# Optimization experiments

Hardware: AMD Instinct MI355X
Metric: run time of the kernel (lower is better)

## Reference

```python
import jax, jax.numpy as jnp
import numpy as np

B, T, D = 1024, 512, 64   # batch, seq_len, input_dim
H, L, OUT = 8, 3, 1       # hidden (mid_dim), num_layers, output_dim


def setup_inputs() -> dict:
    key = jax.random.key(0)
    ks = jax.random.split(key, 18)
    s = 1.0 / np.sqrt(H)  # torch LSTM default init scale
    u = lambda k, shape: jax.random.uniform(k, shape, jnp.float32, -s, s)
    return {
        "input_seq": jax.random.normal(ks[0], (B, T, D), jnp.float32),
        "h0": jax.random.normal(ks[1], (L, B, H), jnp.float32),
        "c0": jax.random.normal(ks[2], (L, B, H), jnp.float32),
        # encoder LSTM params (layer0 input dim differs)
        "enc_Wih0": u(ks[3], (4 * H, D)),
        "enc_Wih_rest": u(ks[4], (L - 1, 4 * H, H)),
        "enc_Whh": u(ks[5], (L, 4 * H, H)),
        "enc_bih": u(ks[6], (L, 4 * H)),
        "enc_bhh": u(ks[7], (L, 4 * H)),
        # decoder LSTM params
        "dec_Wih0": u(ks[8], (4 * H, D)),
        "dec_Wih_rest": u(ks[9], (L - 1, 4 * H, H)),
        "dec_Whh": u(ks[10], (L, 4 * H, H)),
        "dec_bih": u(ks[11], (L, 4 * H)),
        "dec_bhh": u(ks[12], (L, 4 * H)),
        # decoder output projection
        "lin_W": u(ks[13], (OUT, H)),
        "lin_b": u(ks[14], (OUT,)),
    }


def _cell(x, h, c, Wih, Whh, b):
    # one LSTM cell step, torch gate order: i, f, g, o
    gates = x @ Wih.T + h @ Whh.T + b  # [B, 4H]
    i, f, g, o = jnp.split(gates, 4, axis=-1)
    c2 = jax.nn.sigmoid(f) * c + jax.nn.sigmoid(i) * jnp.tanh(g)
    h2 = jax.nn.sigmoid(o) * jnp.tanh(c2)
    return h2, c2


def _stack_step(h, c, x_t, Wih0, Wih_rest, Whh, bih, bhh):
    # one timestep through all L layers; h, c: [L, B, H]
    hs, cs = [], []
    inp = x_t
    for l in range(L):
        Wih = Wih0 if l == 0 else Wih_rest[l - 1]
        h_l, c_l = _cell(inp, h[l], c[l], Wih, Whh[l], bih[l] + bhh[l])
        hs.append(h_l)
        cs.append(c_l)
        inp = h_l
    return jnp.stack(hs), jnp.stack(cs)


def reference(input_seq, h0, c0, enc_Wih0, enc_Wih_rest, enc_Whh, enc_bih, enc_bhh,
              dec_Wih0, dec_Wih_rest, dec_Whh, dec_bih, dec_bhh, lin_W, lin_b):
    x_tbd = jnp.transpose(input_seq, (1, 0, 2))  # [T, B, D] for scan

    # Encoder: full-sequence 3-layer LSTM, keep final (h, c)
    def enc_step(carry, x_t):
        h, c = carry
        h2, c2 = _stack_step(h, c, x_t, enc_Wih0, enc_Wih_rest, enc_Whh, enc_bih, enc_bhh)
        return (h2, c2), None

    (h, c), _ = jax.lax.scan(enc_step, (h0, c0), x_tbd)

    # Decoder: one LSTM step per timestep, fed the input at that step
    def dec_step(carry, x_t):
        h, c = carry
        h2, c2 = _stack_step(h, c, x_t, dec_Wih0, dec_Wih_rest, dec_Whh, dec_bih, dec_bhh)
        return (h2, c2), None

    (h, c), _ = jax.lax.scan(dec_step, (h, c), x_tbd)

    # original returns outputs[:, -1, :] = linear applied to last decoder output
    pred_last = h[-1] @ lin_W.T + lin_b  # [B, OUT]
    return pred_last
```

## Files before the change

### kernel.cpp

```cpp
#include <hip/hip_runtime.h>

#define TT 512
#define DD 64
#define BB 1024
#define PF 8
#define HH 8

__device__ __forceinline__ float fexp2(float x){ return __builtin_amdgcn_exp2f(x); }
__device__ __forceinline__ float frcp (float x){ return __builtin_amdgcn_rcpf(x); }

template<int C>
__device__ __forceinline__ float dppf(float x){
  return __int_as_float(__builtin_amdgcn_update_dpp(0, __float_as_int(x), C, 0xF, 0xF, true));
}
template<int C>
__device__ __forceinline__ int dppi(int x){
  return __builtin_amdgcn_update_dpp(0, x, C, 0xF, 0xF, true);
}

__device__ __forceinline__ float swz16(float x){
  return __int_as_float(__builtin_amdgcn_ds_swizzle(__float_as_int(x), 0x401F));
}

template<int N> struct IC { static constexpr int v = N; };

__global__ __launch_bounds__(256) void proj_kernel(
    const float* __restrict__ x,
    const float* __restrict__ eWih0, const float* __restrict__ eBih, const float* __restrict__ eBhh,
    const float* __restrict__ dWih0, const float* __restrict__ dBih, const float* __restrict__ dBhh,
    float* __restrict__ P)
{
  __shared__ __align__(16) float xs[4][2][16 * 64];
  const int tid  = threadIdx.x;
  const int w    = tid >> 6;
  const int lane = tid & 63;
  const int rsel = lane >> 5;
  const int j    = lane & 31;
  const int ph   = j >> 4;
  const int m    = j & 15;
  const int r_even = (m >> 2) * 8 + (m & 3);
  const int r_odd  = r_even + 4;

  const float* W  = ph ? dWih0 : eWih0;
  const float* Bi = ph ? dBih  : eBih;
  const float* Bh = ph ? dBhh  : eBhh;
  const float bA = Bi[r_even] + Bh[r_even];
  const float bB = Bi[r_odd]  + Bh[r_odd];

  float Wa[64], Wb[64];
#pragma unroll
  for (int k = 0; k < 16; ++k) {
    float4 wq = *(const float4*)(W + r_even * 64 + k * 4);
    Wa[k*4+0] = wq.x; Wa[k*4+1] = wq.y; Wa[k*4+2] = wq.z; Wa[k*4+3] = wq.w;
  }
#pragma unroll
  for (int k = 0; k < 16; ++k) {
    float4 wq = *(const float4*)(W + r_odd * 64 + k * 4);
    Wb[k*4+0] = wq.x; Wb[k*4+1] = wq.y; Wb[k*4+2] = wq.z; Wb[k*4+3] = wq.w;
  }

  const int base_row = (blockIdx.x * 4 + w) * 64;
  const float* xg = x + (size_t)base_row * 64;

  float4 st[4];
#pragma unroll
  for (int i = 0; i < 4; ++i) st[i] = *(const float4*)(xg + i * 256 + lane * 4);
#pragma unroll
  for (int i = 0; i < 4; ++i) *(float4*)&xs[w][0][i * 256 + lane * 4] = st[i];
#pragma unroll
  for (int i = 0; i < 4; ++i) st[i] = *(const float4*)(xg + 1024 + i * 256 + lane * 4);

#pragma unroll 1
  for (int g = 0; g < 4; ++g) {
    const float* buf = &xs[w][g & 1][0];
#pragma unroll 2
    for (int ci = 0; ci < 8; ++ci) {
      const int rib = ci * 2 + rsel;
      const float* xr = buf + rib * 64;
      float a0A = bA, a1A = 0.f, a2A = 0.f, a3A = 0.f;
      float a0B = bB, a1B = 0.f, a2B = 0.f, a3B = 0.f;
#pragma unroll
      for (int kc = 0; kc < 16; ++kc) {
        float4 xv = *(const float4*)(xr + kc * 4);
        a0A = fmaf(Wa[kc*4+0], xv.x, a0A);
        a1A = fmaf(Wa[kc*4+1], xv.y, a1A);
        a2A = fmaf(Wa[kc*4+2], xv.z, a2A);
        a3A = fmaf(Wa[kc*4+3], xv.w, a3A);
        a0B = fmaf(Wb[kc*4+0], xv.x, a0B);
        a1B = fmaf(Wb[kc*4+1], xv.y, a1B);
        a2B = fmaf(Wb[kc*4+2], xv.z, a2B);
        a3B = fmaf(Wb[kc*4+3], xv.w, a3B);
      }
      const int row = base_row + g * 16 + rib;
      const int e = row >> 9, t = row & 511;
      float2 res; res.x = (a0A + a1A) + (a2A + a3A);
                  res.y = (a0B + a1B) + (a2B + a3B);
      *(float2*)(P + ((size_t)((ph << 10) + e) * TT + t) * 32 + 2 * m) = res;
    }
    if (g < 3) {
#pragma unroll
      for (int i = 0; i < 4; ++i) *(float4*)&xs[w][(g + 1) & 1][i * 256 + lane * 4] = st[i];
      if (g < 2) {
#pragma unroll
        for (int i = 0; i < 4; ++i)
          st[i] = *(const float4*)(xg + (size_t)(g + 2) * 1024 + i * 256 + lane * 4);
      }
    }
  }
}

__global__ __launch_bounds__(128) void recur_kernel(
    const float* __restrict__ P,
    const float* __restrict__ h0,    const float* __restrict__ c0,
    const float* __restrict__ eWihR, const float* __restrict__ eWhh,
    const float* __restrict__ eBih,  const float* __restrict__ eBhh,
    const float* __restrict__ dWihR, const float* __restrict__ dWhh,
    const float* __restrict__ dBih,  const float* __restrict__ dBhh,
    const float* __restrict__ linW,  const float* __restrict__ linB,
    float* __restrict__ out)
{
  const int tid = threadIdx.x;
  const int idx = tid & 31;
  const int v   = idx >> 2;
  const int g   = idx & 3;
  const int b   = v & 3;
  const bool rB = (v >= 4);
  const int e   = blockIdx.x * 4 + (tid >> 5);

  const bool is_tanh = (g == 2);
  const float ns_act = is_tanh ? -2.885390082f : -1.44269504f;
  const float a_act  = is_tanh ? 2.0f : 1.0f;
  const float b_act  = is_tanh ? -1.0f : 0.0f;

  const int qidx = (tid >> 2) & 3;
  const int p4 = dppi<0x124>(qidx);
  const int d  = __builtin_amdgcn_readfirstlane((p4 - qidx) & 3);

  float H[3], cs[3], sd[3];
  float bd1 = 0.f, bd2 = 0.f;
  float WS[3][8], WB[2][8], Bss[2];

#pragma unroll
  for (int l = 0; l < 3; ++l) {
    H[l]  = h0[((size_t)l * BB + e) * HH + v];
    cs[l] = c0[((size_t)l * BB + e) * HH + v];
  }

  auto bcast = [&](float hn, float* A, float* Bv) {
    float Hsw = swz16(hn);
    float Lo = rB ? Hsw : hn;
    float Hi = rB ? hn : Hsw;
    A[0]  = Lo; A[1]  = dppf<0x124>(Lo); A[2]  = dppf<0x128>(Lo); A[3]  = dppf<0x12C>(Lo);
    Bv[0] = Hi; Bv[1] = dppf<0x124>(Hi); Bv[2] = dppf<0x128>(Hi); Bv[3] = dppf<0x12C>(Hi);
  };

  auto load_phase = [&](const float* WihR, const float* Whh,
                        const float* Bih, const float* Bhh) {
#pragma unroll
    for (int l = 0; l < 3; ++l) {
      const int r0 = l * 32 + g * 8 + v;
#pragma unroll
      for (int k = 0; k < 4; ++k) {
        const int col = (b + d * k) & 3;
        WS[l][k]     = Whh[r0 * 8 + col];
        WS[l][4 + k] = Whh[r0 * 8 + 4 + col];
      }
    }
#pragma unroll
    for (int l = 0; l < 2; ++l) {
      const int r0 = l * 32 + g * 8 + v;
#pragma unroll
      for (int k = 0; k < 4; ++k) {
        const int col = (b + d * k) & 3;
        WB[l][k]     = WihR[r0 * 8 + col];
        WB[l][4 + k] = WihR[r0 * 8 + 4 + col];
      }
      Bss[l] = Bih[(l + 1) * 32 + g * 8 + v] + Bhh[(l + 1) * 32 + g * 8 + v];
    }
#pragma unroll
    for (int l = 0; l < 3; ++l) {
      float A[4], Bv[4];
      bcast(H[l], A, Bv);
      float acc = l ? Bss[l - 1] : 0.f;
#pragma unroll
      for (int k = 0; k < 4; ++k) {
        acc = fmaf(WS[l][k],     A[k],  acc);
        acc = fmaf(WS[l][4 + k], Bv[k], acc);
      }
      sd[l] = acc;
    }
  };

  auto lstep = [&](auto LC, float in) -> float {
    constexpr int l = decltype(LC)::v;
    float pre = in + sd[l];
    float ex  = fexp2(ns_act * pre);
    float rc  = frcp(1.f + ex);
    float act = fmaf(a_act, rc, b_act);
    float Gi = dppf<0x00>(act);
    float Gf = dppf<0x55>(act);
    float Gg = dppf<0xAA>(act);
    float Go = dppf<0xFF>(act);
    float cn = fmaf(Gf, cs[l], Gi * Gg);
    cs[l] = cn;
    float tx = fexp2(-2.885390082f * cn);
    float tr = frcp(1.f + tx);
    float th = fmaf(2.f, tr, -1.f);
    float hn = Go * th;
    H[l] = hn;
    float A[4], Bv[4];
    bcast(hn, A, Bv);
    float accS;
    if constexpr (l > 0) accS = Bss[l - 1]; else accS = 0.f;
#pragma unroll
    for (int k = 0; k < 4; ++k) {
      accS = fmaf(WS[l][k],     A[k],  accS);
      accS = fmaf(WS[l][4 + k], Bv[k], accS);
    }
    sd[l] = accS;
    float accB = 0.f;
    if constexpr (l < 2) {
#pragma unroll
      for (int k = 0; k < 4; ++k) {
        accB = fmaf(WB[l][k],     A[k],  accB);
        accB = fmaf(WB[l][4 + k], Bv[k], accB);
      }
    }
    return accB;
  };

  auto lstep3 = [&](float in0, float in1, float in2, float& nb1, float& nb2) {
    float pre0 = in0 + sd[0];
    float pre1 = in1 + sd[1];
    float pre2 = in2 + sd[2];
    float ex0 = fexp2(ns_act * pre0);
    float ex1 = fexp2(ns_act * pre1);
    float ex2 = fexp2(ns_act * pre2);
    float rc0 = frcp(1.f + ex0);
    float rc1 = frcp(1.f + ex1);
    float rc2 = frcp(1.f + ex2);
    float ac0 = fmaf(a_act, rc0, b_act);
    float ac1 = fmaf(a_act, rc1, b_act);
    float ac2 = fmaf(a_act, rc2, b_act);
    float Gi0 = dppf<0x00>(ac0), Gi1 = dppf<0x00>(ac1), Gi2 = dppf<0x00>(ac2);
    float Gf0 = dppf<0x55>(ac0), Gf1 = dppf<0x55>(ac1), Gf2 = dppf<0x55>(ac2);
    float Gg0 = dppf<0xAA>(ac0), Gg1 = dppf<0xAA>(ac1), Gg2 = dppf<0xAA>(ac2);
    float Go0 = dppf<0xFF>(ac0), Go1 = dppf<0xFF>(ac1), Go2 = dppf<0xFF>(ac2);
    float cn0 = fmaf(Gf0, cs[0], Gi0 * Gg0);
    float cn1 = fmaf(Gf1, cs[1], Gi1 * Gg1);
    float cn2 = fmaf(Gf2, cs[2], Gi2 * Gg2);
    cs[0] = cn0; cs[1] = cn1; cs[2] = cn2;
    float tx0 = fexp2(-2.885390082f * cn0);
    float tx1 = fexp2(-2.885390082f * cn1);
    float tx2 = fexp2(-2.885390082f * cn2);
    float tr0 = frcp(1.f + tx0);
    float tr1 = frcp(1.f + tx1);
    float tr2 = frcp(1.f + tx2);
    float th0 = fmaf(2.f, tr0, -1.f);
    float th1 = fmaf(2.f, tr1, -1.f);
    float th2 = fmaf(2.f, tr2, -1.f);
    float hn0 = Go0 * th0;
    float hn1 = Go1 * th1;
    float hn2 = Go2 * th2;
    H[0] = hn0; H[1] = hn1; H[2] = hn2;
    float sw0 = swz16(hn0);
    float sw1 = swz16(hn1);
    float sw2 = swz16(hn2);
    float Lo0 = rB ? sw0 : hn0, Hi0 = rB ? hn0 : sw0;
    float Lo1 = rB ? sw1 : hn1, Hi1 = rB ? hn1 : sw1;
    float Lo2 = rB ? sw2 : hn2, Hi2 = rB ? hn2 : sw2;
    float A0[4], B0[4], A1[4], B1[4], A2[4], B2[4];
    A0[0] = Lo0; A0[1] = dppf<0x124>(Lo0); A0[2] = dppf<0x128>(Lo0); A0[3] = dppf<0x12C>(Lo0);
    B0[0] = Hi0; B0[1] = dppf<0x124>(Hi0); B0[2] = dppf<0x128>(Hi0); B0[3] = dppf<0x12C>(Hi0);
    A1[0] = Lo1; A1[1] = dppf<0x124>(Lo1); A1[2] = dppf<0x128>(Lo1); A1[3] = dppf<0x12C>(Lo1);
    B1[0] = Hi1; B1[1] = dppf<0x124>(Hi1); B1[2] = dppf<0x128>(Hi1); B1[3] = dppf<0x12C>(Hi1);
    A2[0] = Lo2; A2[1] = dppf<0x124>(Lo2); A2[2] = dppf<0x128>(Lo2); A2[3] = dppf<0x12C>(Lo2);
    B2[0] = Hi2; B2[1] = dppf<0x124>(Hi2); B2[2] = dppf<0x128>(Hi2); B2[3] = dppf<0x12C>(Hi2);
    float s0 = 0.f, s1 = Bss[0], s2 = Bss[1];
    float u0 = 0.f, u1 = 0.f;
#pragma unroll
    for (int k = 0; k < 4; ++k) {
      s0 = fmaf(WS[0][k],     A0[k], s0);
      s0 = fmaf(WS[0][4 + k], B0[k], s0);
      s1 = fmaf(WS[1][k],     A1[k], s1);
      s1 = fmaf(WS[1][4 + k], B1[k], s1);
      s2 = fmaf(WS[2][k],     A2[k], s2);
      s2 = fmaf(WS[2][4 + k], B2[k], s2);
      u0 = fmaf(WB[0][k],     A0[k], u0);
      u0 = fmaf(WB[0][4 + k], B0[k], u0);
      u1 = fmaf(WB[1][k],     A1[k], u1);
      u1 = fmaf(WB[1][4 + k], B1[k], u1);
    }
    sd[0] = s0; sd[1] = s1; sd[2] = s2;
    nb1 = u0; nb2 = u1;
  };

#pragma unroll 1
  for (int ph = 0; ph < 2; ++ph) {
    if (ph == 0) load_phase(eWihR, eWhh, eBih, eBhh);
    else         load_phase(dWihR, dWhh, dBih, dBhh);

    const int pos = (g * 4 + b) * 2 + (v >> 2);
    const float* Pb = P + ((size_t)((ph << 10) + e) * TT) * 32 + pos;

    float pf[PF];
#pragma unroll
    for (int k = 0; k < PF; ++k) pf[k] = Pb[k * 32];

#pragma unroll
    for (int k = 0; k < PF; ++k) {
      float cur = pf[k];
      pf[k] = Pb[(k + PF) * 32];
      float n1 = lstep(IC<0>{}, cur);
      float n2 = 0.f;
      if (k >= 1) n2 = lstep(IC<1>{}, bd1);
      if (k >= 2) (void)lstep(IC<2>{}, bd2);
      bd1 = n1; bd2 = n2;
    }

#pragma unroll 1
    for (int t = PF; t < TT - PF; t += PF) {
      const float* Pq = Pb + (size_t)(t + PF) * 32;
#pragma unroll
      for (int k = 0; k < PF; ++k) {
        float cur = pf[k];
        pf[k] = Pq[k * 32];
        float n1, n2;
        lstep3(cur, bd1, bd2, n1, n2);
        bd1 = n1; bd2 = n2;
      }
    }
#pragma unroll
    for (int k = 0; k < PF; ++k) {
      float cur = pf[k];
      float n1, n2;
      lstep3(cur, bd1, bd2, n1, n2);
      bd1 = n1; bd2 = n2;
    }

    float dd = lstep(IC<1>{}, bd1);
    (void)lstep(IC<2>{}, bd2);
    (void)lstep(IC<2>{}, dd);
  }

  float lwA[4], lwB[4];
#pragma unroll
  for (int k = 0; k < 4; ++k) {
    const int col = (b + d * k) & 3;
    lwA[k] = linW[col];
    lwB[k] = linW[4 + col];
  }
  float A[4], Bv[4];
  bcast(H[2], A, Bv);
  float pred = linB[0];
#pragma unroll
  for (int k = 0; k < 4; ++k) {
    pred = fmaf(lwA[k], A[k],  pred);
    pred = fmaf(lwB[k], Bv[k], pred);
  }
  if (idx == 0) out[e] = pred;
}

__global__ __launch_bounds__(64) void seq2seq_fallback(
    const float* __restrict__ x, const float* __restrict__ h0, const float* __restrict__ c0,
    const float* __restrict__ eWih0, const float* __restrict__ eWihR, const float* __restrict__ eWhh,
    const float* __restrict__ eBih,  const float* __restrict__ eBhh,
    const float* __restrict__ dWih0, const float* __restrict__ dWihR, const float* __restrict__ dWhh,
    const float* __restrict__ dBih,  const float* __restrict__ dBhh,
    const float* __restrict__ linW,  const float* __restrict__ linB, float* __restrict__ out)
{
  const int tid = threadIdx.x;
  const int g   = tid & 31;
  const int grp = tid & 32;
  const int jj  = g & 7;
  const int e   = blockIdx.x * 2 + (tid >> 5);
  const bool is_tanh = ((g >> 3) == 2);
  const float s_act = is_tanh ? 2.885390082f : 1.44269504f;
  const float a_act = is_tanh ? 2.0f : 1.0f;
  const float b_act = is_tanh ? -1.0f : 0.0f;
  float hrep[3][8]; float cc[3];
#pragma unroll
  for (int l = 0; l < 3; ++l) {
#pragma unroll
    for (int k = 0; k < 8; ++k) hrep[l][k] = h0[((size_t)l * BB + e) * HH + k];
    cc[l] = c0[((size_t)l * BB + e) * HH + jj];
  }
  for (int p = 0; p < 2; ++p) {
    const float* Wih0 = p ? dWih0 : eWih0;  const float* WihR = p ? dWihR : eWihR;
    const float* Whh  = p ? dWhh  : eWhh;   const float* Bih  = p ? dBih  : eBih;
    const float* Bhh  = p ? dBhh  : eBhh;
    float Wx[64];
#pragma unroll
    for (int k = 0; k < 64; k += 4) {
      float4 w = *(const float4*)(Wih0 + g * 64 + k);
      Wx[k] = w.x; Wx[k+1] = w.y; Wx[k+2] = w.z; Wx[k+3] = w.w;
    }
    float Wh[3][8], Wi[2][8], bias[3];
#pragma unroll
    for (int l = 0; l < 3; ++l) {
#pragma unroll
      for (int k = 0; k < 8; ++k) Wh[l][k] = Whh[(l*32+g)*8+k];
      bias[l] = Bih[l*32+g] + Bhh[l*32+g];
    }
#pragma unroll
    for (int l = 0; l < 2; ++l)
#pragma unroll
      for (int k = 0; k < 8; ++k) Wi[l][k] = WihR[(l*32+g)*8+k];
    const float* xrow = x + (size_t)e * TT * DD;
    for (int t = 0; t < TT; ++t) {
      float4 acc = make_float4(bias[0], 0.f, 0.f, 0.f);
#pragma unroll
      for (int kc = 0; kc < 16; ++kc) {
        float4 xv = *(const float4*)(xrow + kc * 4);
        acc.x = fmaf(Wx[kc*4+0], xv.x, acc.x); acc.y = fmaf(Wx[kc*4+1], xv.y, acc.y);
        acc.z = fmaf(Wx[kc*4+2], xv.z, acc.z); acc.w = fmaf(Wx[kc*4+3], xv.w, acc.w);
      }
      float pre = (acc.x + acc.y) + (acc.z + acc.w);
      { float r0=0.f,r1=0.f;
#pragma unroll
        for (int k = 0; k < 8; k += 2) { r0=fmaf(Wh[0][k],hrep[0][k],r0); r1=fmaf(Wh[0][k+1],hrep[0][k+1],r1); }
        pre += r0 + r1; }
#pragma unroll
      for (int l = 0; l < 3; ++l) {
        if (l > 0) {
          float r0 = bias[l], r1 = 0.f;
#pragma unroll
          for (int k = 0; k < 8; k += 2) {
            r0=fmaf(Wi[l-1][k],hrep[l-1][k],r0); r1=fmaf(Wi[l-1][k+1],hrep[l-1][k+1],r1);
            r0=fmaf(Wh[l][k],hrep[l][k],r0);     r1=fmaf(Wh[l][k+1],hrep[l][k+1],r1);
          }
          pre = r0 + r1;
        }
        float act = fmaf(a_act, frcp(1.0f + fexp2(-s_act * pre)), b_act);
        float iv = __shfl(act, grp + jj);
        float fv = __shfl(act, grp + 8 + jj);
        float gv = __shfl(act, grp + 16 + jj);
        float ov = __shfl(act, grp + 24 + jj);
        float cn = fmaf(fv, cc[l], iv * gv);
        cc[l] = cn;
        float th = fmaf(2.0f, frcp(1.0f + fexp2(-2.885390082f * cn)), -1.0f);
        float hn = ov * th;
#pragma unroll
        for (int k = 0; k < 8; ++k) hrep[l][k] = __shfl(hn, grp + k);
      }
      xrow += DD;
    }
  }
  float pred = linB[0];
#pragma unroll
  for (int k = 0; k < 8; ++k) pred = fmaf(linW[k], hrep[2][k], pred);
  if (g == 0) out[e] = pred;
}

extern "C" void kernel_launch(void* const* d_in, const int* in_sizes, int n_in,
                              void* d_out, int out_size, void* d_ws, size_t ws_size,
                              hipStream_t stream) {
  const float* x     = (const float*)d_in[0];
  const float* h0    = (const float*)d_in[1];
  const float* c0    = (const float*)d_in[2];
  const float* eWih0 = (const float*)d_in[3];
  const float* eWihR = (const float*)d_in[4];
  const float* eWhh  = (const float*)d_in[5];
  const float* eBih  = (const float*)d_in[6];
  const float* eBhh  = (const float*)d_in[7];
  const float* dWih0 = (const float*)d_in[8];
  const float* dWihR = (const float*)d_in[9];
  const float* dWhh  = (const float*)d_in[10];
  const float* dBih  = (const float*)d_in[11];
  const float* dBhh  = (const float*)d_in[12];
  const float* linW  = (const float*)d_in[13];
  const float* linB  = (const float*)d_in[14];
  float* out = (float*)d_out;

  const size_t P_BYTES = (size_t)2 * BB * TT * 32 * sizeof(float);
  if (ws_size >= P_BYTES) {
    float* P = (float*)d_ws;
    proj_kernel<<<2048, 256, 0, stream>>>(x, eWih0, eBih, eBhh, dWih0, dBih, dBhh, P);
    recur_kernel<<<BB / 4, 128, 0, stream>>>(P, h0, c0, eWihR, eWhh, eBih, eBhh,
                                             dWihR, dWhh, dBih, dBhh, linW, linB, out);
  } else {
    seq2seq_fallback<<<BB / 2, 64, 0, stream>>>(x, h0, c0, eWih0, eWihR, eWhh, eBih, eBhh,
                                                dWih0, dWihR, dWhh, dBih, dBhh, linW, linB, out);
  }
}
```

Measured before the change: 573.8 us.

## Fuse input projection into recurrence kernel with producer/consumer waves via LDS

Replaces the separate projection kernel and its global workspace with one fused kernel. Two waves per block compute the layer-0 input projection for 32-timestep windows into double-buffered LDS, while the other two waves run the LSTM recurrence, with a block barrier at each window boundary. This removes the large global write and read-back of the projected gates and one kernel launch. The cost is 96KB of LDS per block, a barrier every window, and consumer waves that may stall if producers fall behind. The fallback kernel is removed.

```diff
diff --git a/kernel.cpp b/kernel.cpp
--- a/kernel.cpp
+++ b/kernel.cpp
@@ -5,6 +5,8 @@
 #define BB 1024
 #define PF 8
 #define HH 8
+#define WBLK 32
+#define NWIN (TT / WBLK)
 
 __device__ __forceinline__ float fexp2(float x){ return __builtin_amdgcn_exp2f(x); }
 __device__ __forceinline__ float frcp (float x){ return __builtin_amdgcn_rcpf(x); }
@@ -24,108 +26,32 @@
 
 template<int N> struct IC { static constexpr int v = N; };
 
-__global__ __launch_bounds__(256) void proj_kernel(
+__global__ __launch_bounds__(256) void fused_kernel(
     const float* __restrict__ x,
-    const float* __restrict__ eWih0, const float* __restrict__ eBih, const float* __restrict__ eBhh,
-    const float* __restrict__ dWih0, const float* __restrict__ dBih, const float* __restrict__ dBhh,
-    float* __restrict__ P)
-{
-  __shared__ __align__(16) float xs[4][2][16 * 64];
-  const int tid  = threadIdx.x;
-  const int w    = tid >> 6;
-  const int lane = tid & 63;
-  const int rsel = lane >> 5;
-  const int j    = lane & 31;
-  const int ph   = j >> 4;
-  const int m    = j & 15;
-  const int r_even = (m >> 2) * 8 + (m & 3);
-  const int r_odd  = r_even + 4;
-
-  const float* W  = ph ? dWih0 : eWih0;
-  const float* Bi = ph ? dBih  : eBih;
-  const float* Bh = ph ? dBhh  : eBhh;
-  const float bA = Bi[r_even] + Bh[r_even];
-  const float bB = Bi[r_odd]  + Bh[r_odd];
-
-  float Wa[64], Wb[64];
-#pragma unroll
-  for (int k = 0; k < 16; ++k) {
-    float4 wq = *(const float4*)(W + r_even * 64 + k * 4);
-    Wa[k*4+0] = wq.x; Wa[k*4+1] = wq.y; Wa[k*4+2] = wq.z; Wa[k*4+3] = wq.w;
-  }
-#pragma unroll
-  for (int k = 0; k < 16; ++k) {
-    float4 wq = *(const float4*)(W + r_odd * 64 + k * 4);
-    Wb[k*4+0] = wq.x; Wb[k*4+1] = wq.y; Wb[k*4+2] = wq.z; Wb[k*4+3] = wq.w;
-  }
-
-  const int base_row = (blockIdx.x * 4 + w) * 64;
-  const float* xg = x + (size_t)base_row * 64;
-
-  float4 st[4];
-#pragma unroll
-  for (int i = 0; i < 4; ++i) st[i] = *(const float4*)(xg + i * 256 + lane * 4);
-#pragma unroll
-  for (int i = 0; i < 4; ++i) *(float4*)&xs[w][0][i * 256 + lane * 4] = st[i];
-#pragma unroll
-  for (int i = 0; i < 4; ++i) st[i] = *(const float4*)(xg + 1024 + i * 256 + lane * 4);
-
-#pragma unroll 1
-  for (int g = 0; g < 4; ++g) {
-    const float* buf = &xs[w][g & 1][0];
-#pragma unroll 2
-    for (int ci = 0; ci < 8; ++ci) {
-      const int rib = ci * 2 + rsel;
-      const float* xr = buf + rib * 64;
-      float a0A = bA, a1A = 0.f, a2A = 0.f, a3A = 0.f;
-      float a0B = bB, a1B = 0.f, a2B = 0.f, a3B = 0.f;
-#pragma unroll
-      for (int kc = 0; kc < 16; ++kc) {
-        float4 xv = *(const float4*)(xr + kc * 4);
-        a0A = fmaf(Wa[kc*4+0], xv.x, a0A);
-        a1A = fmaf(Wa[kc*4+1], xv.y, a1A);
-        a2A = fmaf(Wa[kc*4+2], xv.z, a2A);
-        a3A = fmaf(Wa[kc*4+3], xv.w, a3A);
-        a0B = fmaf(Wb[kc*4+0], xv.x, a0B);
-        a1B = fmaf(Wb[kc*4+1], xv.y, a1B);
-        a2B = fmaf(Wb[kc*4+2], xv.z, a2B);
-        a3B = fmaf(Wb[kc*4+3], xv.w, a3B);
-      }
-      const int row = base_row + g * 16 + rib;
-      const int e = row >> 9, t = row & 511;
-      float2 res; res.x = (a0A + a1A) + (a2A + a3A);
-                  res.y = (a0B + a1B) + (a2B + a3B);
-      *(float2*)(P + ((size_t)((ph << 10) + e) * TT + t) * 32 + 2 * m) = res;
-    }
-    if (g < 3) {
-#pragma unroll
-      for (int i = 0; i < 4; ++i) *(float4*)&xs[w][(g + 1) & 1][i * 256 + lane * 4] = st[i];
-      if (g < 2) {
-#pragma unroll
-        for (int i = 0; i < 4; ++i)
-          st[i] = *(const float4*)(xg + (size_t)(g + 2) * 1024 + i * 256 + lane * 4);
-      }
-    }
-  }
-}
-
-__global__ __launch_bounds__(128) void recur_kernel(
-    const float* __restrict__ P,
     const float* __restrict__ h0,    const float* __restrict__ c0,
-    const float* __restrict__ eWihR, const float* __restrict__ eWhh,
+    const float* __restrict__ eWih0, const float* __restrict__ eWihR, const float* __restrict__ eWhh,
     const float* __restrict__ eBih,  const float* __restrict__ eBhh,
-    const float* __restrict__ dWihR, const float* __restrict__ dWhh,
+    const float* __restrict__ dWih0, const float* __restrict__ dWihR, const float* __restrict__ dWhh,
     const float* __restrict__ dBih,  const float* __restrict__ dBhh,
     const float* __restrict__ linW,  const float* __restrict__ linB,
     float* __restrict__ out)
 {
-  const int tid = threadIdx.x;
+  extern __shared__ __align__(16) float smem[];
+  float* Pbuf = smem;
+  float* xst  = smem + 2 * WBLK * 4 * 32;
+
+  const int tid  = threadIdx.x;
+  const int wv   = tid >> 6;
+  const int lane = tid & 63;
+  const bool prod = (wv >= 2);
+
   const int idx = tid & 31;
   const int v   = idx >> 2;
   const int g   = idx & 3;
   const int b   = v & 3;
   const bool rB = (v >= 4);
-  const int e   = blockIdx.x * 4 + (tid >> 5);
+  const int erow = tid >> 5;
+  const int e    = blockIdx.x * 4 + erow;
 
   const bool is_tanh = (g == 2);
   const float ns_act = is_tanh ? -2.885390082f : -1.44269504f;
@@ -138,13 +64,23 @@
 
   float H[3], cs[3], sd[3];
   float bd1 = 0.f, bd2 = 0.f;
-  float WS[3][8], WB[2][8], Bss[2];
-
-#pragma unroll
-  for (int l = 0; l < 3; ++l) {
-    H[l]  = h0[((size_t)l * BB + e) * HH + v];
-    cs[l] = c0[((size_t)l * BB + e) * HH + v];
+  float WS[3][8], WBr[2][8], Bss[2];
+
+  if (!prod) {
+#pragma unroll
+    for (int l = 0; l < 3; ++l) {
+      H[l]  = h0[((size_t)l * BB + e) * HH + v];
+      cs[l] = c0[((size_t)l * BB + e) * HH + v];
+    }
   }
+
+  const int rsel = lane >> 4;
+  const int m    = lane & 15;
+  const int r_even = (m >> 2) * 8 + (m & 3);
+  const int r_odd  = r_even + 4;
+  const int p0 = (wv - 2) * 2;
+  float Wa[64], Wb[64];
+  float bA = 0.f, bB = 0.f;
 
   auto bcast = [&](float hn, float* A, float* Bv) {
     float Hsw = swz16(hn);
@@ -172,8 +108,8 @@
 #pragma unroll
       for (int k = 0; k < 4; ++k) {
         const int col = (b + d * k) & 3;
-        WB[l][k]     = WihR[r0 * 8 + col];
-        WB[l][4 + k] = WihR[r0 * 8 + 4 + col];
+        WBr[l][k]     = WihR[r0 * 8 + col];
+        WBr[l][4 + k] = WihR[r0 * 8 + 4 + col];
       }
       Bss[l] = Bih[(l + 1) * 32 + g * 8 + v] + Bhh[(l + 1) * 32 + g * 8 + v];
     }
@@ -222,8 +158,8 @@
     if constexpr (l < 2) {
 #pragma unroll
       for (int k = 0; k < 4; ++k) {
-        accB = fmaf(WB[l][k],     A[k],  accB);
-        accB = fmaf(WB[l][4 + k], Bv[k], accB);
+        accB = fmaf(WBr[l][k],     A[k],  accB);
+        accB = fmaf(WBr[l][4 + k], Bv[k], accB);
       }
     }
     return accB;
@@ -286,170 +222,163 @@
       s1 = fmaf(WS[1][4 + k], B1[k], s1);
       s2 = fmaf(WS[2][k],     A2[k], s2);
       s2 = fmaf(WS[2][4 + k], B2[k], s2);
-      u0 = fmaf(WB[0][k],     A0[k], u0);
-      u0 = fmaf(WB[0][4 + k], B0[k], u0);
-      u1 = fmaf(WB[1][k],     A1[k], u1);
-      u1 = fmaf(WB[1][4 + k], B1[k], u1);
+      u0 = fmaf(WBr[0][k],     A0[k], u0);
+      u0 = fmaf(WBr[0][4 + k], B0[k], u0);
+      u1 = fmaf(WBr[1][k],     A1[k], u1);
+      u1 = fmaf(WBr[1][4 + k], B1[k], u1);
     }
     sd[0] = s0; sd[1] = s1; sd[2] = s2;
     nb1 = u0; nb2 = u1;
   };
 
-#pragma unroll 1
-  for (int ph = 0; ph < 2; ++ph) {
-    if (ph == 0) load_phase(eWihR, eWhh, eBih, eBhh);
-    else         load_phase(dWihR, dWhh, dBih, dBhh);
-
-    const int pos = (g * 4 + b) * 2 + (v >> 2);
-    const float* Pb = P + ((size_t)((ph << 10) + e) * TT) * 32 + pos;
-
+  const int pos_c = (g * 4 + b) * 2 + (v >> 2);
+
+  auto consume = [&](int w) {
+    const float* Pw = Pbuf + ((w & 1) * WBLK * 4 * 32) + erow * 32 + pos_c;
     float pf[PF];
 #pragma unroll
-    for (int k = 0; k < PF; ++k) pf[k] = Pb[k * 32];
-
-#pragma unroll
-    for (int k = 0; k < PF; ++k) {
-      float cur = pf[k];
-      pf[k] = Pb[(k + PF) * 32];
-      float n1 = lstep(IC<0>{}, cur);
-      float n2 = 0.f;
-      if (k >= 1) n2 = lstep(IC<1>{}, bd1);
-      if (k >= 2) (void)lstep(IC<2>{}, bd2);
-      bd1 = n1; bd2 = n2;
-    }
-
-#pragma unroll 1
-    for (int t = PF; t < TT - PF; t += PF) {
-      const float* Pq = Pb + (size_t)(t + PF) * 32;
+    for (int k = 0; k < PF; ++k) pf[k] = Pw[k * 128];
+    if (w == 0) {
 #pragma unroll
       for (int k = 0; k < PF; ++k) {
         float cur = pf[k];
-        pf[k] = Pq[k * 32];
-        float n1, n2;
-        lstep3(cur, bd1, bd2, n1, n2);
+        pf[k] = Pw[(PF + k) * 128];
+        float n1 = lstep(IC<0>{}, cur);
+        float n2 = 0.f;
+        if (k >= 1) n2 = lstep(IC<1>{}, bd1);
+        if (k >= 2) (void)lstep(IC<2>{}, bd2);
         bd1 = n1; bd2 = n2;
       }
-    }
-#pragma unroll
-    for (int k = 0; k < PF; ++k) {
-      float cur = pf[k];
+#pragma unroll 1
+      for (int gi = 1; gi < 3; ++gi) {
+#pragma unroll
+        for (int j = 0; j < PF; ++j) {
+          float cur = pf[j];
+          pf[j] = Pw[((gi + 1) * PF + j) * 128];
+          float n1, n2;
+          lstep3(cur, bd1, bd2, n1, n2);
+          bd1 = n1; bd2 = n2;
+        }
+      }
+    } else {
+#pragma unroll 1
+      for (int gi = 0; gi < 3; ++gi) {
+#pragma unroll
+        for (int j = 0; j < PF; ++j) {
+          float cur = pf[j];
+          pf[j] = Pw[((gi + 1) * PF + j) * 128];
+          float n1, n2;
+          lstep3(cur, bd1, bd2, n1, n2);
+          bd1 = n1; bd2 = n2;
+        }
+      }
+    }
+#pragma unroll
+    for (int j = 0; j < PF; ++j) {
+      float cur = pf[j];
       float n1, n2;
       lstep3(cur, bd1, bd2, n1, n2);
       bd1 = n1; bd2 = n2;
     }
-
-    float dd = lstep(IC<1>{}, bd1);
-    (void)lstep(IC<2>{}, bd2);
-    (void)lstep(IC<2>{}, dd);
+  };
+
+  auto produce = [&](int w, int buf) {
+#pragma unroll 1
+    for (int es = 0; es < 2; ++es) {
+      const int p  = p0 + es;
+      const float* xg = x + ((size_t)(blockIdx.x * 4 + p) * TT + w * WBLK) * 64;
+      float* xp = xst + p * (WBLK * 64);
+      float4 sv[8];
+#pragma unroll
+      for (int i = 0; i < 8; ++i) sv[i] = *(const float4*)(xg + i * 256 + lane * 4);
+#pragma unroll
+      for (int i = 0; i < 8; ++i) *(float4*)(xp + i * 256 + lane * 4) = sv[i];
+#pragma unroll 1
+      for (int ci = 0; ci < 8; ++ci) {
+        const int rib = ci * 4 + rsel;
+        const float* xr = xp + rib * 64;
+        float a0A = bA, a1A = 0.f, a2A = 0.f, a3A = 0.f;
+        float a0B = bB, a1B = 0.f, a2B = 0.f, a3B = 0.f;
+#pragma unroll
+        for (int kc = 0; kc < 16; ++kc) {
+          float4 xv = *(const float4*)(xr + kc * 4);
+          a0A = fmaf(Wa[kc*4+0], xv.x, a0A);
+          a1A = fmaf(Wa[kc*4+1], xv.y, a1A);
+          a2A = fmaf(Wa[kc*4+2], xv.z, a2A);
+          a3A = fmaf(Wa[kc*4+3], xv.w, a3A);
+          a0B = fmaf(Wb[kc*4+0], xv.x, a0B);
+          a1B = fmaf(Wb[kc*4+1], xv.y, a1B);
+          a2B = fmaf(Wb[kc*4+2], xv.z, a2B);
+          a3B = fmaf(Wb[kc*4+3], xv.w, a3B);
+        }
+        float2 res;
+        res.x = (a0A + a1A) + (a2A + a3A);
+        res.y = (a0B + a1B) + (a2B + a3B);
+        *(float2*)(Pbuf + ((size_t)(buf * WBLK + rib) * 4 + p) * 32 + 2 * m) = res;
+      }
+    }
+  };
+
+#pragma unroll 1
+  for (int ph = 0; ph < 2; ++ph) {
+    if (prod) {
+      const float* W  = ph ? dWih0 : eWih0;
+      const float* Bi = ph ? dBih  : eBih;
+      const float* Bh = ph ? dBhh  : eBhh;
+      bA = Bi[r_even] + Bh[r_even];
+      bB = Bi[r_odd]  + Bh[r_odd];
+#pragma unroll
+      for (int k = 0; k < 16; ++k) {
+        float4 wq = *(const float4*)(W + r_even * 64 + k * 4);
+        Wa[k*4+0] = wq.x; Wa[k*4+1] = wq.y; Wa[k*4+2] = wq.z; Wa[k*4+3] = wq.w;
+      }
+#pragma unroll
+      for (int k = 0; k < 16; ++k) {
+        float4 wq = *(const float4*)(W + r_odd * 64 + k * 4);
+        Wb[k*4+0] = wq.x; Wb[k*4+1] = wq.y; Wb[k*4+2] = wq.z; Wb[k*4+3] = wq.w;
+      }
+      produce(0, 0);
+    } else {
+      if (ph == 0) load_phase(eWihR, eWhh, eBih, eBhh);
+      else         load_phase(dWihR, dWhh, dBih, dBhh);
+    }
+    __syncthreads();
+
+#pragma unroll 1
+    for (int w = 0; w < NWIN; ++w) {
+      if (prod) {
+        if (w < NWIN - 1) produce(w + 1, (w + 1) & 1);
+      } else {
+        consume(w);
+      }
+      __syncthreads();
+    }
+
+    if (!prod) {
+      float dd = lstep(IC<1>{}, bd1);
+      (void)lstep(IC<2>{}, bd2);
+      (void)lstep(IC<2>{}, dd);
+    }
   }
 
-  float lwA[4], lwB[4];
-#pragma unroll
-  for (int k = 0; k < 4; ++k) {
-    const int col = (b + d * k) & 3;
-    lwA[k] = linW[col];
-    lwB[k] = linW[4 + col];
+  if (!prod) {
+    float lwA[4], lwB[4];
+#pragma unroll
+    for (int k = 0; k < 4; ++k) {
+      const int col = (b + d * k) & 3;
+      lwA[k] = linW[col];
+      lwB[k] = linW[4 + col];
+    }
+    float A[4], Bv[4];
+    bcast(H[2], A, Bv);
+    float pred = linB[0];
+#pragma unroll
+    for (int k = 0; k < 4; ++k) {
+      pred = fmaf(lwA[k], A[k],  pred);
+      pred = fmaf(lwB[k], Bv[k], pred);
+    }
+    if (idx == 0) out[e] = pred;
   }
-  float A[4], Bv[4];
-  bcast(H[2], A, Bv);
-  float pred = linB[0];
-#pragma unroll
-  for (int k = 0; k < 4; ++k) {
-    pred = fmaf(lwA[k], A[k],  pred);
-    pred = fmaf(lwB[k], Bv[k], pred);
-  }
-  if (idx == 0) out[e] = pred;
-}
-
-__global__ __launch_bounds__(64) void seq2seq_fallback(
-    const float* __restrict__ x, const float* __restrict__ h0, const float* __restrict__ c0,
-    const float* __restrict__ eWih0, const float* __restrict__ eWihR, const float* __restrict__ eWhh,
-    const float* __restrict__ eBih,  const float* __restrict__ eBhh,
-    const float* __restrict__ dWih0, const float* __restrict__ dWihR, const float* __restrict__ dWhh,
-    const float* __restrict__ dBih,  const float* __restrict__ dBhh,
-    const float* __restrict__ linW,  const float* __restrict__ linB, float* __restrict__ out)
-{
-  const int tid = threadIdx.x;
-  const int g   = tid & 31;
-  const int grp = tid & 32;
-  const int jj  = g & 7;
-  const int e   = blockIdx.x * 2 + (tid >> 5);
-  const bool is_tanh = ((g >> 3) == 2);
-  const float s_act = is_tanh ? 2.885390082f : 1.44269504f;
-  const float a_act = is_tanh ? 2.0f : 1.0f;
-  const float b_act = is_tanh ? -1.0f : 0.0f;
-  float hrep[3][8]; float cc[3];
-#pragma unroll
-  for (int l = 0; l < 3; ++l) {
-#pragma unroll
-    for (int k = 0; k < 8; ++k) hrep[l][k] = h0[((size_t)l * BB + e) * HH + k];
-    cc[l] = c0[((size_t)l * BB + e) * HH + jj];
-  }
-  for (int p = 0; p < 2; ++p) {
-    const float* Wih0 = p ? dWih0 : eWih0;  const float* WihR = p ? dWihR : eWihR;
-    const float* Whh  = p ? dWhh  : eWhh;   const float* Bih  = p ? dBih  : eBih;
-    const float* Bhh  = p ? dBhh  : eBhh;
-    float Wx[64];
-#pragma unroll
-    for (int k = 0; k < 64; k += 4) {
-      float4 w = *(const float4*)(Wih0 + g * 64 + k);
-      Wx[k] = w.x; Wx[k+1] = w.y; Wx[k+2] = w.z; Wx[k+3] = w.w;
-    }
-    float Wh[3][8], Wi[2][8], bias[3];
-#pragma unroll
-    for (int l = 0; l < 3; ++l) {
-#pragma unroll
-      for (int k = 0; k < 8; ++k) Wh[l][k] = Whh[(l*32+g)*8+k];
-      bias[l] = Bih[l*32+g] + Bhh[l*32+g];
-    }
-#pragma unroll
-    for (int l = 0; l < 2; ++l)
-#pragma unroll
-      for (int k = 0; k < 8; ++k) Wi[l][k] = WihR[(l*32+g)*8+k];
-    const float* xrow = x + (size_t)e * TT * DD;
-    for (int t = 0; t < TT; ++t) {
-      float4 acc = make_float4(bias[0], 0.f, 0.f, 0.f);
-#pragma unroll
-      for (int kc = 0; kc < 16; ++kc) {
-        float4 xv = *(const float4*)(xrow + kc * 4);
-        acc.x = fmaf(Wx[kc*4+0], xv.x, acc.x); acc.y = fmaf(Wx[kc*4+1], xv.y, acc.y);
-        acc.z = fmaf(Wx[kc*4+2], xv.z, acc.z); acc.w = fmaf(Wx[kc*4+3], xv.w, acc.w);
-      }
-      float pre = (acc.x + acc.y) + (acc.z + acc.w);
-      { float r0=0.f,r1=0.f;
-#pragma unroll
-        for (int k = 0; k < 8; k += 2) { r0=fmaf(Wh[0][k],hrep[0][k],r0); r1=fmaf(Wh[0][k+1],hrep[0][k+1],r1); }
-        pre += r0 + r1; }
-#pragma unroll
-      for (int l = 0; l < 3; ++l) {
-        if (l > 0) {
-          float r0 = bias[l], r1 = 0.f;
-#pragma unroll
-          for (int k = 0; k < 8; k += 2) {
-            r0=fmaf(Wi[l-1][k],hrep[l-1][k],r0); r1=fmaf(Wi[l-1][k+1],hrep[l-1][k+1],r1);
-            r0=fmaf(Wh[l][k],hrep[l][k],r0);     r1=fmaf(Wh[l][k+1],hrep[l][k+1],r1);
-          }
-          pre = r0 + r1;
-        }
-        float act = fmaf(a_act, frcp(1.0f + fexp2(-s_act * pre)), b_act);
-        float iv = __shfl(act, grp + jj);
-        float fv = __shfl(act, grp + 8 + jj);
-        float gv = __shfl(act, grp + 16 + jj);
-        float ov = __shfl(act, grp + 24 + jj);
-        float cn = fmaf(fv, cc[l], iv * gv);
-        cc[l] = cn;
-        float th = fmaf(2.0f, frcp(1.0f + fexp2(-2.885390082f * cn)), -1.0f);
-        float hn = ov * th;
-#pragma unroll
-        for (int k = 0; k < 8; ++k) hrep[l][k] = __shfl(hn, grp + k);
-      }
-      xrow += DD;
-    }
-  }
-  float pred = linB[0];
-#pragma unroll
-  for (int k = 0; k < 8; ++k) pred = fmaf(linW[k], hrep[2][k], pred);
-  if (g == 0) out[e] = pred;
 }
 
 extern "C" void kernel_launch(void* const* d_in, const int* in_sizes, int n_in,
@@ -472,14 +401,7 @@
   const float* linB  = (const float*)d_in[14];
   float* out = (float*)d_out;
 
-  const size_t P_BYTES = (size_t)2 * BB * TT * 32 * sizeof(float);
-  if (ws_size >= P_BYTES) {
-    float* P = (float*)d_ws;
-    proj_kernel<<<2048, 256, 0, stream>>>(x, eWih0, eBih, eBhh, dWih0, dBih, dBhh, P);
-    recur_kernel<<<BB / 4, 128, 0, stream>>>(P, h0, c0, eWihR, eWhh, eBih, eBhh,
-                                             dWihR, dWhh, dBih, dBhh, linW, linB, out);
-  } else {
-    seq2seq_fallback<<<BB / 2, 64, 0, stream>>>(x, h0, c0, eWih0, eWihR, eWhh, eBih, eBhh,
-                                                dWih0, dWihR, dWhh, dBih, dBhh, linW, linB, out);
-  }
+  fused_kernel<<<BB / 4, 256, 98304, stream>>>(
+      x, h0, c0, eWih0, eWihR, eWhh, eBih, eBhh,
+      dWih0, dWihR, dWhh, dBih, dBhh, linW, linB, out);
 }
```

After: 521.0 us. 1.1x faster.
